# Optimization experiments

Measured on AMD Instinct MI355X. Metric: run time of the kernel, lower is better.

## Reference

```python
import jax, jax.numpy as jnp
import numpy as np

N_NODES = 50000
N_EDGES = 800000
IN_DIM = 128
HIDDEN = 256
N_CLASSES = 16
N_GRAPHS = 128


def setup_inputs() -> dict:
    key = jax.random.key(0)
    ks = jax.random.split(key, 10)
    x = jax.random.normal(ks[0], (N_NODES, IN_DIM), dtype=jnp.float32)
    edge_index = jax.random.randint(ks[1], (2, N_EDGES), 0, N_NODES, dtype=jnp.int64)
    batch = jnp.sort(jax.random.randint(ks[2], (N_NODES,), 0, N_GRAPHS, dtype=jnp.int64))
    s = 1.0 / np.sqrt(HIDDEN)
    return {
        "x": x,
        "edge_index": edge_index,
        "batch": batch,
        "W_in": jax.random.normal(ks[3], (IN_DIM, HIDDEN), dtype=jnp.float32) / np.sqrt(IN_DIM),
        "b_in": jnp.zeros((HIDDEN,), dtype=jnp.float32),
        "W1": jax.random.normal(ks[4], (HIDDEN, HIDDEN), dtype=jnp.float32) * s,
        "b1": jnp.zeros((HIDDEN,), dtype=jnp.float32),
        "W2": jax.random.normal(ks[5], (HIDDEN, HIDDEN), dtype=jnp.float32) * s,
        "b2": jnp.zeros((HIDDEN,), dtype=jnp.float32),
        "W_out": jax.random.normal(ks[6], (HIDDEN, N_CLASSES), dtype=jnp.float32) * s,
        "b_out": jnp.zeros((N_CLASSES,), dtype=jnp.float32),
    }


def gcn_conv(x, W, b, src, dst):
    # PyG GCNConv: add self-loops, symmetric norm D^-1/2 A D^-1/2, scatter-add at target.
    h = x @ W  # [N, H]
    n = x.shape[0]
    # degree of target nodes, including one self-loop per node
    deg = jax.ops.segment_sum(jnp.ones_like(dst, dtype=h.dtype), dst, num_segments=n) + 1.0
    dinv = deg ** -0.5  # [N]
    norm = dinv[src] * dinv[dst]  # [E]
    msg = h[src] * norm[:, None]  # [E, H]  gather + scale
    agg = jax.ops.segment_sum(msg, dst, num_segments=n)  # scatter-add
    agg = agg + h * (dinv * dinv)[:, None]  # self-loop contribution
    return agg + b


def reference(x, edge_index, batch, W_in, b_in, W1, b1, W2, b2, W_out, b_out):
    src, dst = edge_index[0], edge_index[1]
    h = x @ W_in + b_in
    # layer 1 (dropout is identity in eval mode)
    h = jax.nn.relu(gcn_conv(h, W1, b1, src, dst))
    # layer 2
    h = jax.nn.relu(gcn_conv(h, W2, b2, src, dst))
    # global mean pool over graphs
    sums = jax.ops.segment_sum(h, batch, num_segments=N_GRAPHS)  # [G, H]
    counts = jax.ops.segment_sum(jnp.ones((h.shape[0],), h.dtype), batch, num_segments=N_GRAPHS)
    pooled = sums / jnp.maximum(counts, 1.0)[:, None]
    return pooled @ W_out + b_out  # [G, n_classes]
```

## Files before the change

kernel.cpp:

```cpp
#include <hip/hip_runtime.h>
#include <hip/hip_bf16.h>

typedef __attribute__((ext_vector_type(8))) short bf16x8;
typedef __attribute__((ext_vector_type(4))) float f32x4;

__device__ __forceinline__ unsigned short f2bf(float f) {
    unsigned u = __float_as_uint(f);
    u += 0x7fff + ((u >> 16) & 1);
    return (unsigned short)(u >> 16);
}
__device__ __forceinline__ float bf2f(unsigned short s) {
    return __uint_as_float(((unsigned)s) << 16);
}

#define GL2LDS16(g, l) __builtin_amdgcn_global_load_lds(                      \
        (const __attribute__((address_space(1))) void*)(g),                   \
        (__attribute__((address_space(3))) void*)(l), 16, 0, 0)


__global__ __launch_bounds__(256) void fused_misc_kernel(
        const float* __restrict__ W2, unsigned short* __restrict__ Wt2,
        const float* __restrict__ x, unsigned short* __restrict__ xb, int n4,
        const float* __restrict__ W_in, const float* __restrict__ b_in,
        const float* __restrict__ W1,
        unsigned short* __restrict__ WfT, float* __restrict__ bv,
        const int* __restrict__ src, const int* __restrict__ dst,
        int* __restrict__ cursor, unsigned short* __restrict__ csr16,
        unsigned short* __restrict__ zrow,
        float* __restrict__ sums, int* __restrict__ counts,
        int e, int FB, int WB) {
    __shared__ float row[256];
    __shared__ unsigned short tile[64][65];
    int b = blockIdx.x;
    if (b < FB) {
        int i = b * 256 + threadIdx.x;
        if (i < e) {
            int d = dst[i];
            int p = atomicAdd(&cursor[d], 1);
            if (p < 64) csr16[((size_t)d << 6) + p] = (unsigned short)src[i];
        }
    } else if (b < FB + WB) {
        int k = b - FB;
        int nn = threadIdx.x;
        row[nn] = (k < 128) ? W_in[k * 256 + nn] : b_in[nn];
        __syncthreads();
        float acc = 0.f;
        #pragma unroll 4
        for (int j = 0; j < 256; ++j) acc = fmaf(row[j], W1[j * 256 + nn], acc);
        if (k < 128) WfT[(size_t)nn * 128 + k] = f2bf(acc);
        else bv[nn] = acc;
    } else if (b < FB + WB + 16) {
        int t = b - FB - WB;
        int ti = t >> 2, tj = t & 3;
        int rq = threadIdx.x >> 4;
        int c0 = (threadIdx.x & 15) * 4;
        #pragma unroll
        for (int rr = 0; rr < 64; rr += 16) {
            int r = rr + rq;
            float4 v = *(const float4*)&W2[(size_t)(ti * 64 + r) * 256 + tj * 64 + c0];
            tile[r][c0]     = f2bf(v.x);
            tile[r][c0 + 1] = f2bf(v.y);
            tile[r][c0 + 2] = f2bf(v.z);
            tile[r][c0 + 3] = f2bf(v.w);
        }
        __syncthreads();
        #pragma unroll
        for (int rr = 0; rr < 64; rr += 16) {
            int nrow = rr + rq;
            ushort4 o;
            o.x = tile[c0][nrow];
            o.y = tile[c0 + 1][nrow];
            o.z = tile[c0 + 2][nrow];
            o.w = tile[c0 + 3][nrow];
            *(ushort4*)&Wt2[(size_t)(tj * 64 + nrow) * 256 + ti * 64 + c0] = o;
        }
    } else if (b == FB + WB + 16) {
        if (threadIdx.x < 128) ((unsigned*)zrow)[threadIdx.x] = 0u;
    } else if (b < FB + WB + 16 + 1 + 129) {
        int j = b - (FB + WB + 17);
        if (j < 128) sums[j * 256 + threadIdx.x] = 0.f;
        else if (threadIdx.x < 128) counts[threadIdx.x] = 0;
    } else {
        int i = (b - FB - WB - 17 - 129) * 256 + threadIdx.x;
        if (i < n4) {
            float4 v = ((const float4*)x)[i];
            ushort4 o;
            o.x = f2bf(v.x); o.y = f2bf(v.y); o.z = f2bf(v.z); o.w = f2bf(v.w);
            ((ushort4*)xb)[i] = o;
        }
    }
}


template <int MODE>
__global__ __launch_bounds__(512) void gemm_bf16(const unsigned short* __restrict__ A,
                                                 const unsigned short* __restrict__ Wt,
                                                 const float* __restrict__ aux,
                                                 const float* __restrict__ aux2,
                                                 const float* __restrict__ aux3,
                                                 unsigned short* __restrict__ C,
                                                 int M, int K) {
    __shared__ unsigned short S[3072 * 8];
    const int tid  = threadIdx.x;
    const int lane = tid & 63;
    const int w    = tid >> 6;
    const int wr   = w >> 2, wc = w & 3;
    const int row0 = blockIdx.x * 128;
    const int mlane = lane & 15, quad = lane >> 4;

    f32x4 acc[4][4];
    #pragma unroll
    for (int i = 0; i < 4; ++i)
        #pragma unroll
        for (int j = 0; j < 4; ++j) acc[i][j] = f32x4{0.f, 0.f, 0.f, 0.f};

    const unsigned short* g[6]; unsigned short* l[6];
    #pragma unroll
    for (int q = 0; q < 6; ++q) {
        int cid = q * 512 + tid;
        l[q] = &S[(q * 512 + w * 64) * 8];
        if (cid < 1024) {
            int r = cid >> 3, slot = cid & 7;
            int rowA = row0 + r; if (rowA >= M) rowA = M - 1;
            g[q] = A + (size_t)rowA * K + slot * 8;
        } else {
            int j = cid - 1024;
            int col = j >> 3, slot = j & 7;
            g[q] = Wt + (size_t)col * K + slot * 8;
        }
    }

    for (int k0 = 0; k0 < K; k0 += 64) {
        #pragma unroll
        for (int q = 0; q < 6; ++q) GL2LDS16(g[q] + k0, l[q]);
        __syncthreads();
        #pragma unroll
        for (int ks = 0; ks < 2; ++ks) {
            bf16x8 af[4], bfv[4];
            #pragma unroll
            for (int i = 0; i < 4; ++i)
                af[i] = *(const bf16x8*)&S[(wr * 64 + i * 16 + mlane) * 64 + ks * 32 + quad * 8];
            #pragma unroll
            for (int j = 0; j < 4; ++j)
                bfv[j] = *(const bf16x8*)&S[8192 + (wc * 64 + j * 16 + mlane) * 64 + ks * 32 + quad * 8];
            #pragma unroll
            for (int i = 0; i < 4; ++i)
                #pragma unroll
                for (int j = 0; j < 4; ++j)
                    acc[i][j] = __builtin_amdgcn_mfma_f32_16x16x32_bf16(af[i], bfv[j], acc[i][j], 0, 0, 0);
        }
        __syncthreads();
    }

    float bj[4], cj[4];
    if (MODE == 0) {
        #pragma unroll
        for (int j = 0; j < 4; ++j) bj[j] = aux[wc * 64 + j * 16 + mlane];
    } else if (MODE == 2) {
        #pragma unroll
        for (int j = 0; j < 4; ++j) {
            int gcol = wc * 64 + j * 16 + mlane;
            bj[j] = aux2[gcol];
            cj[j] = aux3[gcol];
        }
    }
    #pragma unroll
    for (int i = 0; i < 4; ++i) {
        #pragma unroll
        for (int r = 0; r < 4; ++r) {
            int grow = row0 + wr * 64 + i * 16 + quad * 4 + r;
            if (grow < M) {
                float d = 0.f;
                if (MODE == 1) d = rsqrtf((float)((const int*)aux)[grow] + 1.0f);
                else if (MODE == 2) d = aux[grow];
                #pragma unroll
                for (int j = 0; j < 4; ++j) {
                    int gcol = wc * 64 + j * 16 + mlane;
                    float v = acc[i][j][r];
                    if (MODE == 0)      v = v + bj[j];
                    else if (MODE == 1) v = v * d;
                    else {              v = fmaf(d, bj[j], v) + cj[j]; v = fmaxf(v, 0.f); }
                    C[(size_t)grow * 256 + gcol] = f2bf(v);
                }
            }
        }
    }
}


__global__ __launch_bounds__(256) void agg_x_kernel(const unsigned short* __restrict__ xb,
                                                    const int* __restrict__ deg,
                                                    const unsigned short* __restrict__ csr16,
                                                    unsigned short* __restrict__ ax,
                                                    float* __restrict__ s_out, int n) {
    int node = blockIdx.x * 4 + (threadIdx.x >> 6);
    if (node >= n) return;
    int lane = threadIdx.x & 63;
    int half = lane >> 5, hl = lane & 31;
    const ushort4* x4 = (const ushort4*)xb;
    int cnt = deg[node]; if (cnt > 64) cnt = 64;
    size_t beg = (size_t)node << 6;
    float dn = rsqrtf((float)deg[node] + 1.0f);
    float a0 = 0.f, a1 = 0.f, a2 = 0.f, a3 = 0.f;
    float sdl = 0.f;

    int myi = 0; float mydv = 0.f;
    if (lane < cnt) {
        myi = (int)csr16[beg + lane];
        mydv = rsqrtf((float)deg[myi] + 1.0f);
        sdl += mydv;
    }
    for (int j = 0; j < cnt; j += 8) {
        int s0 = __shfl(myi, j + half),     s1 = __shfl(myi, j + 2 + half);
        int s2 = __shfl(myi, j + 4 + half), s3 = __shfl(myi, j + 6 + half);
        float d0 = __shfl(mydv, j + half),     d1 = __shfl(mydv, j + 2 + half);
        float d2 = __shfl(mydv, j + 4 + half), d3 = __shfl(mydv, j + 6 + half);
        ushort4 v0 = x4[(size_t)s0 * 32 + hl];
        ushort4 v1 = x4[(size_t)s1 * 32 + hl];
        ushort4 v2 = x4[(size_t)s2 * 32 + hl];
        ushort4 v3 = x4[(size_t)s3 * 32 + hl];
        a0 = fmaf(bf2f(v0.x), d0, a0); a1 = fmaf(bf2f(v0.y), d0, a1);
        a2 = fmaf(bf2f(v0.z), d0, a2); a3 = fmaf(bf2f(v0.w), d0, a3);
        a0 = fmaf(bf2f(v1.x), d1, a0); a1 = fmaf(bf2f(v1.y), d1, a1);
        a2 = fmaf(bf2f(v1.z), d1, a2); a3 = fmaf(bf2f(v1.w), d1, a3);
        a0 = fmaf(bf2f(v2.x), d2, a0); a1 = fmaf(bf2f(v2.y), d2, a1);
        a2 = fmaf(bf2f(v2.z), d2, a2); a3 = fmaf(bf2f(v2.w), d2, a3);
        a0 = fmaf(bf2f(v3.x), d3, a0); a1 = fmaf(bf2f(v3.y), d3, a1);
        a2 = fmaf(bf2f(v3.z), d3, a2); a3 = fmaf(bf2f(v3.w), d3, a3);
    }

    a0 += __shfl_xor(a0, 32); a1 += __shfl_xor(a1, 32);
    a2 += __shfl_xor(a2, 32); a3 += __shfl_xor(a3, 32);
    float sd = sdl;
    #pragma unroll
    for (int off = 32; off > 0; off >>= 1) sd += __shfl_down(sd, off);
    if (lane < 32) {
        ushort4 sv = x4[(size_t)node * 32 + hl];
        a0 = fmaf(dn, bf2f(sv.x), a0) * dn;
        a1 = fmaf(dn, bf2f(sv.y), a1) * dn;
        a2 = fmaf(dn, bf2f(sv.z), a2) * dn;
        a3 = fmaf(dn, bf2f(sv.w), a3) * dn;
        ushort4 r;
        r.x = f2bf(a0); r.y = f2bf(a1); r.z = f2bf(a2); r.w = f2bf(a3);
        ((ushort4*)ax)[(size_t)node * 32 + hl] = r;
        if (lane == 0) s_out[node] = dn * (sd + dn);
    }
}


__global__ __launch_bounds__(256) void agg_kernel(const unsigned short* __restrict__ hs,
                                                  const int* __restrict__ deg,
                                                  const unsigned short* __restrict__ csr16,
                                                  const float* __restrict__ bias,
                                                  unsigned short* __restrict__ out, int n) {
    int node = blockIdx.x * 4 + (threadIdx.x >> 6);
    if (node >= n) return;
    int lane = threadIdx.x & 63;
    const ushort4* hs4 = (const ushort4*)hs;
    int cnt = deg[node]; if (cnt > 64) cnt = 64;
    size_t beg = (size_t)node << 6;
    ushort4 sv = hs4[(size_t)node * 64 + lane];
    float a0 = bf2f(sv.x), a1 = bf2f(sv.y), a2 = bf2f(sv.z), a3 = bf2f(sv.w);
    float c0 = 0.f, c1 = 0.f, c2 = 0.f, c3 = 0.f;

    int myi = (lane < cnt) ? (int)csr16[beg + lane] : n;
    for (int j = 0; j < cnt; j += 8) {
        int s0 = __shfl(myi, j + 0), s1 = __shfl(myi, j + 1);
        int s2 = __shfl(myi, j + 2), s3 = __shfl(myi, j + 3);
        int s4 = __shfl(myi, j + 4), s5 = __shfl(myi, j + 5);
        int s6 = __shfl(myi, j + 6), s7 = __shfl(myi, j + 7);
        ushort4 v0 = hs4[(size_t)s0 * 64 + lane];
        ushort4 v1 = hs4[(size_t)s1 * 64 + lane];
        ushort4 v2 = hs4[(size_t)s2 * 64 + lane];
        ushort4 v3 = hs4[(size_t)s3 * 64 + lane];
        ushort4 v4 = hs4[(size_t)s4 * 64 + lane];
        ushort4 v5 = hs4[(size_t)s5 * 64 + lane];
        ushort4 v6 = hs4[(size_t)s6 * 64 + lane];
        ushort4 v7 = hs4[(size_t)s7 * 64 + lane];
        a0 += bf2f(v0.x) + bf2f(v1.x) + bf2f(v2.x) + bf2f(v3.x);
        a1 += bf2f(v0.y) + bf2f(v1.y) + bf2f(v2.y) + bf2f(v3.y);
        a2 += bf2f(v0.z) + bf2f(v1.z) + bf2f(v2.z) + bf2f(v3.z);
        a3 += bf2f(v0.w) + bf2f(v1.w) + bf2f(v2.w) + bf2f(v3.w);
        c0 += bf2f(v4.x) + bf2f(v5.x) + bf2f(v6.x) + bf2f(v7.x);
        c1 += bf2f(v4.y) + bf2f(v5.y) + bf2f(v6.y) + bf2f(v7.y);
        c2 += bf2f(v4.z) + bf2f(v5.z) + bf2f(v6.z) + bf2f(v7.z);
        c3 += bf2f(v4.w) + bf2f(v5.w) + bf2f(v6.w) + bf2f(v7.w);
    }
    a0 += c0; a1 += c1; a2 += c2; a3 += c3;

    float d = rsqrtf((float)deg[node] + 1.0f);
    float4 b = ((const float4*)bias)[lane];
    ushort4 r;
    r.x = f2bf(fmaxf(fmaf(a0, d, b.x), 0.f));
    r.y = f2bf(fmaxf(fmaf(a1, d, b.y), 0.f));
    r.z = f2bf(fmaxf(fmaf(a2, d, b.z), 0.f));
    r.w = f2bf(fmaxf(fmaf(a3, d, b.w), 0.f));
    ((ushort4*)out)[(size_t)node * 64 + lane] = r;
}


__global__ __launch_bounds__(256) void pool_partial_kernel(const unsigned short* __restrict__ h,
                                                           const int* __restrict__ batch,
                                                           float* __restrict__ sums,
                                                           int* __restrict__ counts,
                                                           int n, int chunk) {
    int beg = blockIdx.x * chunk;
    int end = beg + chunk; if (end > n) end = n;
    if (beg >= end) return;
    int c = threadIdx.x;
    int curg = batch[beg];
    float acc = 0.f;
    int runlen = 0;
    for (int i = beg; i < end; ++i) {
        int g = batch[i];
        if (g != curg) {
            atomicAdd(&sums[(size_t)curg * 256 + c], acc);
            if (c == 0) atomicAdd(&counts[curg], runlen);
            acc = 0.f; runlen = 0; curg = g;
        }
        acc += bf2f(h[(size_t)i * 256 + c]);
        ++runlen;
    }
    atomicAdd(&sums[(size_t)curg * 256 + c], acc);
    if (c == 0) atomicAdd(&counts[curg], runlen);
}

__global__ __launch_bounds__(256) void pool_final_kernel(const float* __restrict__ sums,
                                                         const int* __restrict__ counts,
                                                         const float* __restrict__ Wout,
                                                         const float* __restrict__ bout,
                                                         float* __restrict__ out) {
    __shared__ float pl[256];
    int g = blockIdx.x;
    int c = threadIdx.x;
    int cnt = counts[g];
    pl[c] = sums[(size_t)g * 256 + c] / (float)(cnt > 0 ? cnt : 1);
    __syncthreads();
    if (c < 16) {
        float o = bout[c];
        #pragma unroll 4
        for (int k = 0; k < 256; ++k) o = fmaf(pl[k], Wout[k * 16 + c], o);
        out[g * 16 + c] = o;
    }
}


extern "C" void kernel_launch(void* const* d_in, const int* in_sizes, int n_in,
                              void* d_out, int out_size, void* d_ws, size_t ws_size,
                              hipStream_t stream) {
    const float* x     = (const float*)d_in[0];
    const int*   ei    = (const int*)d_in[1];
    const int*   batch = (const int*)d_in[2];
    const float* W_in  = (const float*)d_in[3];
    const float* b_in  = (const float*)d_in[4];
    const float* W1    = (const float*)d_in[5];
    const float* b1    = (const float*)d_in[6];
    const float* W2    = (const float*)d_in[7];
    const float* b2    = (const float*)d_in[8];
    const float* Wout  = (const float*)d_in[9];
    const float* bout  = (const float*)d_in[10];

    const int E = in_sizes[1] / 2;
    const int N = in_sizes[2];
    const int IN_DIM = in_sizes[0] / N;
    const int G = 128;
    const int* src = ei;
    const int* dst = ei + E;

    char* ws = (char*)d_ws;
    size_t off = 0;
    auto alloc = [&](size_t bytes) { size_t p = off; off += (bytes + 255) & ~(size_t)255; return p; };
    unsigned short* bufA = (unsigned short*)(ws + alloc((size_t)N * 256 * 2));
    unsigned short* bufB = (unsigned short*)(ws + alloc((size_t)(N + 1) * 256 * 2));
    unsigned short* xb   = (unsigned short*)(ws + alloc((size_t)N * IN_DIM * 2));
    unsigned short* Wt2  = (unsigned short*)(ws + alloc((size_t)256 * 256 * 2));
    unsigned short* WfT  = (unsigned short*)(ws + alloc((size_t)256 * IN_DIM * 2));
    float*          bv   = (float*)(ws + alloc((size_t)256 * 4));
    float*          sbuf = (float*)(ws + alloc((size_t)N * 4));
    float* sums    = (float*)(ws + alloc((size_t)G * 256 * 4));
    int*   counts  = (int*)(ws + alloc((size_t)G * 4));
    size_t zbeg = off;
    int*   cursor  = (int*)(ws + alloc((size_t)N * 4));
    size_t zend = off;
    unsigned short* csr16 = (unsigned short*)(ws + alloc((size_t)N * 64 * 2));
    (void)ws_size;

    unsigned short* axb = bufB;
    unsigned short* zrow = bufB + (size_t)N * 256;

    const int XB  = (N * IN_DIM / 4 + 255) / 256;
    const int WB  = 129;
    const int FB  = (E + 255) / 256;
    const int SB  = 129;
    const int MB  = (N + 127) / 128;

    hipMemsetAsync(ws + zbeg, 0, zend - zbeg, stream);
    fused_misc_kernel<<<FB + WB + 16 + 1 + SB + XB, 256, 0, stream>>>(
        W2, Wt2, x, xb, N * IN_DIM / 4, W_in, b_in, W1, WfT, bv,
        src, dst, cursor, csr16, zrow, sums, counts, E, FB, WB);

    agg_x_kernel<<<(N + 3) / 4, 256, 0, stream>>>(xb, cursor, csr16, axb, sbuf, N);
    gemm_bf16<2><<<MB, 512, 0, stream>>>(axb, WfT, sbuf, bv, b1, bufA, N, IN_DIM);

    gemm_bf16<1><<<MB, 512, 0, stream>>>(bufA, Wt2, (const float*)cursor, nullptr, nullptr, bufB, N, 256);
    agg_kernel<<<(N + 3) / 4, 256, 0, stream>>>(bufB, cursor, csr16, b2, bufA, N);

    const int PBLOCKS = 512;
    int chunk = (N + PBLOCKS - 1) / PBLOCKS;
    pool_partial_kernel<<<PBLOCKS, 256, 0, stream>>>(bufA, batch, sums, counts, N, chunk);
    pool_final_kernel<<<G, 256, 0, stream>>>(sums, counts, Wout, bout, (float*)d_out);
}
```

Baseline: 315.1 us.

## Keep full weight tile resident in LDS and double-buffer A tiles in GEMM

The bf16 GEMM now loads the entire transposed weight matrix (K×256) into shared memory once per block. It then streams 64-row A tiles through a double buffer, prefetching the next K-slice while the MFMAs consume the current one. Block height drops from 128 to 64 rows, so more blocks launch, and K becomes a compile-time template parameter so the loop fully unrolls. The aim is to stop reloading weights every K-step and to overlap A loads with compute. The cost is a much larger LDS footprint per block, especially for K=256, which can limit blocks per CU.

```diff
diff --git a/kernel.cpp b/kernel.cpp
--- a/kernel.cpp
+++ b/kernel.cpp
@@ -92,59 +92,60 @@
 }
 
 
-template <int MODE>
+template <int MODE, int KT>
 __global__ __launch_bounds__(512) void gemm_bf16(const unsigned short* __restrict__ A,
                                                  const unsigned short* __restrict__ Wt,
                                                  const float* __restrict__ aux,
                                                  const float* __restrict__ aux2,
                                                  const float* __restrict__ aux3,
                                                  unsigned short* __restrict__ C,
-                                                 int M, int K) {
-    __shared__ unsigned short S[3072 * 8];
+                                                 int M) {
+    __shared__ unsigned short S[8192 + 256 * KT];
     const int tid  = threadIdx.x;
     const int lane = tid & 63;
     const int w    = tid >> 6;
     const int wr   = w >> 2, wc = w & 3;
-    const int row0 = blockIdx.x * 128;
+    const int row0 = blockIdx.x * 64;
     const int mlane = lane & 15, quad = lane >> 4;
 
-    f32x4 acc[4][4];
+    f32x4 acc[2][4];
     #pragma unroll
-    for (int i = 0; i < 4; ++i)
+    for (int i = 0; i < 2; ++i)
         #pragma unroll
         for (int j = 0; j < 4; ++j) acc[i][j] = f32x4{0.f, 0.f, 0.f, 0.f};
 
-    const unsigned short* g[6]; unsigned short* l[6];
+    constexpr int BPT = (32 * KT) / 512;
     #pragma unroll
-    for (int q = 0; q < 6; ++q) {
+    for (int q = 0; q < BPT; ++q) {
         int cid = q * 512 + tid;
-        l[q] = &S[(q * 512 + w * 64) * 8];
-        if (cid < 1024) {
-            int r = cid >> 3, slot = cid & 7;
-            int rowA = row0 + r; if (rowA >= M) rowA = M - 1;
-            g[q] = A + (size_t)rowA * K + slot * 8;
-        } else {
-            int j = cid - 1024;
-            int col = j >> 3, slot = j & 7;
-            g[q] = Wt + (size_t)col * K + slot * 8;
-        }
-    }
-
-    for (int k0 = 0; k0 < K; k0 += 64) {
-        #pragma unroll
-        for (int q = 0; q < 6; ++q) GL2LDS16(g[q] + k0, l[q]);
-        __syncthreads();
+        int col = cid / (KT / 8), slot = cid % (KT / 8);
+        GL2LDS16(Wt + (size_t)col * KT + slot * 8, &S[8192 + (q * 512 + w * 64) * 8]);
+    }
+    const unsigned short* gA;
+    {
+        int r = tid >> 3, slot = tid & 7;
+        int rowA = row0 + r; if (rowA >= M) rowA = M - 1;
+        gA = A + (size_t)rowA * KT + slot * 8;
+        GL2LDS16(gA, &S[(w * 64) * 8]);
+    }
+    __syncthreads();
+
+    #pragma unroll
+    for (int t = 0; t < KT / 64; ++t) {
+        if (t + 1 < KT / 64)
+            GL2LDS16(gA + (t + 1) * 64, &S[((t + 1) & 1) * 4096 + (w * 64) * 8]);
+        const int abase = (t & 1) * 4096;
         #pragma unroll
         for (int ks = 0; ks < 2; ++ks) {
-            bf16x8 af[4], bfv[4];
+            bf16x8 af[2], bfv[4];
             #pragma unroll
-            for (int i = 0; i < 4; ++i)
-                af[i] = *(const bf16x8*)&S[(wr * 64 + i * 16 + mlane) * 64 + ks * 32 + quad * 8];
+            for (int i = 0; i < 2; ++i)
+                af[i] = *(const bf16x8*)&S[abase + (wr * 32 + i * 16 + mlane) * 64 + ks * 32 + quad * 8];
             #pragma unroll
             for (int j = 0; j < 4; ++j)
-                bfv[j] = *(const bf16x8*)&S[8192 + (wc * 64 + j * 16 + mlane) * 64 + ks * 32 + quad * 8];
+                bfv[j] = *(const bf16x8*)&S[8192 + (wc * 64 + j * 16 + mlane) * KT + t * 64 + ks * 32 + quad * 8];
             #pragma unroll
-            for (int i = 0; i < 4; ++i)
+            for (int i = 0; i < 2; ++i)
                 #pragma unroll
                 for (int j = 0; j < 4; ++j)
                     acc[i][j] = __builtin_amdgcn_mfma_f32_16x16x32_bf16(af[i], bfv[j], acc[i][j], 0, 0, 0);
@@ -165,10 +166,10 @@
         }
     }
     #pragma unroll
-    for (int i = 0; i < 4; ++i) {
+    for (int i = 0; i < 2; ++i) {
         #pragma unroll
         for (int r = 0; r < 4; ++r) {
-            int grow = row0 + wr * 64 + i * 16 + quad * 4 + r;
+            int grow = row0 + wr * 32 + i * 16 + quad * 4 + r;
             if (grow < M) {
                 float d = 0.f;
                 if (MODE == 1) d = rsqrtf((float)((const int*)aux)[grow] + 1.0f);
@@ -392,7 +393,7 @@
     const int WB  = 129;
     const int FB  = (E + 255) / 256;
     const int SB  = 129;
-    const int MB  = (N + 127) / 128;
+    const int MB  = (N + 63) / 64;
 
     hipMemsetAsync(ws + zbeg, 0, zend - zbeg, stream);
     fused_misc_kernel<<<FB + WB + 16 + 1 + SB + XB, 256, 0, stream>>>(
@@ -400,9 +401,9 @@
         src, dst, cursor, csr16, zrow, sums, counts, E, FB, WB);
 
     agg_x_kernel<<<(N + 3) / 4, 256, 0, stream>>>(xb, cursor, csr16, axb, sbuf, N);
-    gemm_bf16<2><<<MB, 512, 0, stream>>>(axb, WfT, sbuf, bv, b1, bufA, N, IN_DIM);
-
-    gemm_bf16<1><<<MB, 512, 0, stream>>>(bufA, Wt2, (const float*)cursor, nullptr, nullptr, bufB, N, 256);
+    gemm_bf16<2, 128><<<MB, 512, 0, stream>>>(axb, WfT, sbuf, bv, b1, bufA, N);
+
+    gemm_bf16<1, 256><<<MB, 512, 0, stream>>>(bufA, Wt2, (const float*)cursor, nullptr, nullptr, bufB, N);
     agg_kernel<<<(N + 3) / 4, 256, 0, stream>>>(bufB, cursor, csr16, b2, bufA, N);
 
     const int PBLOCKS = 512;
```

Result: slower. 332.2 us (+5.4%).
